# Optimization experiments

Measured on AMD Instinct MI355X. Metric: run time of the kernel, lower is better.

## Reference

```python
import jax
import jax.numpy as jnp
import numpy as np
from jax import lax

DELTA = float(np.exp(-2.0))  # rule-creation density threshold


def codebook_lamb(x):
    """Online growing RBF prototype codebook (ALMMo-style) for one layer.

    x: [N, M]. Returns lamb: [N] normalized density of each sample at its
    assigned rule. Faithful (corrected) semantics of Layer.__call__:
      - SEN = squared L2 norm per sample (over feature dim)
      - global mean / mean squared norm over the batch
      - sequential per-sample: if max RBF density over existing rules < exp(-2),
        append a new rule (prototype=c=x, SENc=||x||^2, support=1);
        else update rule_star. Note the source's `support[rule_star] = +1`
        assigns 1, so the running mean update degenerates to c[rule_star]=x,
        SENc[rule_star]=||x||^2 -- replicated here.
      - distances use the (never-updated) prototypes; bandwidth stau uses c.
    """
    N, M = x.shape
    SENx = jnp.sum(x * x, axis=-1)                      # [N]
    gmean = jnp.mean(x, axis=0)                         # [M]
    base = jnp.mean(SENx) - jnp.sum(gmean * gmean)      # SENgmean - SEN(gmean)
    R = N                                               # worst case: one rule/sample

    protos0 = jnp.zeros((R, M), x.dtype)
    pn20 = jnp.zeros((R,), x.dtype)                     # ||proto_r||^2 (carried)
    c0 = jnp.zeros((R, M), x.dtype)
    cn20 = jnp.zeros((R,), x.dtype)                     # ||c_r||^2 (carried)
    SENc0 = jnp.zeros((R,), x.dtype)
    count0 = jnp.int32(0)

    ridx = jnp.arange(R)

    def step(carry, inp):
        protos, pn2, c, cn2, SENc, count = carry
        xi, sxi = inp                                   # [M], scalar
        valid = ridx < count
        stau = (base + SENc - cn2) * 0.5                # [R]
        dist = sxi + pn2 - 2.0 * (protos @ xi)          # [R] ||xi - proto_r||^2
        dens = jnp.where(valid, jnp.exp(-dist / stau), -jnp.inf)
        idx = jnp.argmax(dens)
        vmax = dens[idx]
        new = (count == 0) | (vmax < DELTA)
        slot = jnp.where(new, count, idx)
        # both branches set c/SENc at slot to xi/sxi (support resets to 1)
        c = c.at[slot].set(xi)
        cn2 = cn2.at[slot].set(sxi)
        SENc = SENc.at[slot].set(sxi)
        # only a new rule writes a prototype (OOB scatter when count==R is dropped)
        protos = protos.at[count].set(jnp.where(new, xi, protos[count]))
        pn2 = pn2.at[count].set(jnp.where(new, sxi, pn2[count]))
        count = count + new.astype(count.dtype)
        return (protos, pn2, c, cn2, SENc, count), slot

    (protos, pn2, c, cn2, SENc, count), rules = lax.scan(
        step, (protos0, pn20, c0, cn20, SENc0, count0), (x, SENx)
    )

    # final densities of all samples under all (valid) rules: [R, N]
    stau = (base + SENc - cn2) * 0.5                    # [R]
    dist = SENx[None, :] + pn2[:, None] - 2.0 * (protos @ x.T)
    dens = jnp.where((ridx < count)[:, None], jnp.exp(-dist / stau[:, None]), 0.0)
    dens_xn = dens[rules, jnp.arange(N)]                # density at assigned rule
    lamb = dens_xn / jnp.sum(dens, axis=0)              # normalize over rules
    return lamb


def setup_inputs() -> dict:
    key = jax.random.key(0)
    k = jax.random.split(key, 5)
    N, D_IN, D_H, D_OUT = 2048, 2048, 2048, 1024
    s0 = 1.0 / np.sqrt(D_IN)
    s1 = 1.0 / np.sqrt(D_H)
    return {
        "x": jax.random.normal(k[0], (N, D_IN), jnp.float32),
        "W0": jax.random.normal(k[1], (D_H, D_IN), jnp.float32) * s0,
        "b0": jax.random.normal(k[2], (D_H,), jnp.float32) * s0,
        "W1": jax.random.normal(k[3], (D_OUT, D_H), jnp.float32) * s1,
        "b1": jax.random.normal(k[4], (D_OUT,), jnp.float32) * s1,
    }


def reference(x, W0, b0, W1, b1):
    lambs = []
    h = x
    for W, b in ((W0, b0), (W1, b1)):
        lambs.append(codebook_lamb(h))          # per-layer codebook on layer input
        h = jax.nn.sigmoid(h @ W.T + b)         # torch.nn.Linear + sigmoid
    return h, jnp.stack(lambs)                  # ([N, d_out], [n_layers, N])
```

## Files before the change

### kernel.cpp

```cpp
#include <hip/hip_runtime.h>
#include <cstdint>
#include <cstddef>


#define DELTA_F 0.13533528323661270f
#define MBYTE (1u << 20)

typedef __bf16 bf16;
typedef bf16 bf16x8 __attribute__((ext_vector_type(8)));
typedef bf16 bf16x4 __attribute__((ext_vector_type(4)));
typedef float f32x4 __attribute__((ext_vector_type(4)));

typedef __attribute__((address_space(1))) void as1_void;
typedef __attribute__((address_space(3))) void as3_void;

__device__ __forceinline__ void gload16(const bf16* g, bf16* l) {
  __builtin_amdgcn_global_load_lds((as1_void*)g, (as3_void*)l, 16, 0, 0);
}

__device__ __forceinline__ float wave_reduce(float s) {
  for (int o = 32; o > 0; o >>= 1) s += __shfl_down(s, o, 64);
  return s;
}

template <bool SAME>
__device__ void run_decide_lamb(char* smem, int* e, float* Dens, float* S,
                                float* diagD, float* lambOut) {
  char* s_flag = smem;
  short* s_as = (short*)(smem + 2048);
  short* s_list = (short*)(smem + 6144);
  short* s_re = (short*)(smem + 10240);
  int* scan_ = (int*)(smem + 14336);
  float* rbest = (float*)(smem + 16384);
  int* rbj = (int*)(smem + 18432);
  int* sT = (int*)(smem + 24576);
  int* sReN = (int*)(smem + 24580);
  const int tid = threadIdx.x;
  int cntl = 0;
#pragma unroll
  for (int k = 0; k < 4; ++k) {
    const int i = tid * 4 + k;
    const int ei = SAME ? atomicOr(e + i, 0) : e[i];
    s_flag[i] = (ei == 0);
    if (ei == 0) s_as[i] = (short)i;
    cntl += (ei != 0);
  }
  scan_[tid] = cntl;
  if (tid == 0) sReN[0] = 0;
  __syncthreads();
  for (int off = 1; off < 512; off <<= 1) {
    const int v = scan_[tid];
    const int add = (tid >= off) ? scan_[tid - off] : 0;
    __syncthreads();
    scan_[tid] = v + add;
    __syncthreads();
  }
  int pos = scan_[tid] - cntl;
#pragma unroll
  for (int k = 0; k < 4; ++k) {
    const int i = tid * 4 + k;
    if (!s_flag[i]) s_list[pos++] = (short)i;
  }
  if (tid == 511) sT[0] = scan_[511];
  __syncthreads();
  const int T = sT[0];
  if (SAME && T > 0) __threadfence();
  for (int t = 0; t < T; ++t) {
    const int i = s_list[t];
    const float* di = Dens + (size_t)i * 2048;
    float best = -1.0f;
    int bestj = 0x7fffffff;
    for (int j = tid; j < i; j += 512) {
      if (s_flag[j]) {
        const float d = di[j];
        if (d > best || (d == best && j < bestj)) { best = d; bestj = j; }
      }
    }
    rbest[tid] = best; rbj[tid] = bestj;
    __syncthreads();
    if (tid == 0) {
      float b = -1.0f;
      int bj = 0x7fffffff;
      for (int k = 0; k < 512; ++k)
        if (rbest[k] > b || (rbest[k] == b && rbj[k] < bj)) { b = rbest[k]; bj = rbj[k]; }
      if (b < DELTA_F) { s_flag[i] = 1; s_as[i] = (short)i; }
      else { s_as[i] = (short)bj; s_re[sReN[0]++] = (short)i; }
    }
    __syncthreads();
  }
  const int reN = sReN[0];
#pragma unroll
  for (int k = 0; k < 4; ++k) {
    const int n = k * 512 + tid;
    const int aa = s_as[n];
    const float num = (aa == n)
        ? (SAME ? atomicAdd(diagD + n, 0.f) : diagD[n])
        : Dens[(size_t)n * 2048 + aa];
    float denom = SAME ? atomicAdd(S + n, 0.f) : S[n];
    for (int t = 0; t < reN; ++t) denom -= Dens[(size_t)n * 2048 + s_re[t]];
    lambOut[n] = num / denom;
  }
}

template <bool IS_L0>
__global__ __launch_bounds__(512, 4) void gemm_fused(
    const bf16* __restrict__ A, float* __restrict__ Dens,
    bf16* __restrict__ Hb, float* __restrict__ Fo,
    const float* __restrict__ bias, const float* __restrict__ SENin,
    const float* __restrict__ ninv_p, float* __restrict__ S,
    int* __restrict__ e, float* __restrict__ SENhOut,
    float* __restrict__ colsumH, float* __restrict__ diagD,
    int* __restrict__ cnt, int nblocks, float* __restrict__ lambOut,
    int* __restrict__ flagN, const float* __restrict__ SENh_r,
    const float* __restrict__ colsumH_r, int* __restrict__ e0,
    float* __restrict__ S0, float* __restrict__ diag0,
    float* __restrict__ Dens0, float* __restrict__ lamb0) {
  __shared__ __align__(16) char smem[32768];
  __shared__ int s_last;
  const int tid = threadIdx.x;

  if (!IS_L0 && blockIdx.x == 24) {
    if (blockIdx.y != 0) return;
    float* r1 = (float*)(smem + 20480);
    float* r2 = (float*)(smem + 22528);
    float ssen = 0.f, sg2 = 0.f;
    for (int i = tid; i < 2048; i += 512) ssen += SENh_r[i];
    for (int c = tid; c < 2048; c += 512) {
      const float gm = colsumH_r[c] * (1.f / 2048.f);
      sg2 += gm * gm;
    }
    r1[tid] = ssen; r2[tid] = sg2;
    __syncthreads();
    for (int s = 256; s; s >>= 1) {
      if (tid < s) { r1[tid] += r1[tid + s]; r2[tid] += r2[tid + s]; }
      __syncthreads();
    }
    if (tid == 0) {
      const float stau = 0.5f * (r1[0] * (1.f / 2048.f) - r2[0]);
      atomicExch(flagN, __float_as_int(-1.f / stau));
    }
    __syncthreads();
    run_decide_lamb<false>(smem, e0, Dens0, S0, diag0, lamb0);
    return;
  }

  const int wave = tid >> 6, lane = tid & 63;
  const int quad = lane >> 4, l16 = lane & 15;
  const int kg = wave & 1, wm = (wave >> 1) & 1, wn = (wave >> 2) & 1;
  const int m0 = blockIdx.y * 128, n0 = blockIdx.x * 128;
  const int waveM = wm * 64, waveN = wn * 64;
  const bool isGram = (n0 < 2048);
  const int sr8 = lane >> 3, slot = lane & 7;
  const int gk = (slot ^ sr8) * 8;
  const bf16* aSrc = A + (size_t)(m0 + wave * 16 + sr8) * 2048 + gk;
  const bf16* bSrc = A + (size_t)(n0 + wave * 16 + sr8) * 2048 + gk;
  char* const aDst = smem + wave * 2048;
  char* const bDst = smem + 16384 + wave * 2048;
  const int swz = ((kg * 4 + quad) ^ (l16 & 7)) * 16;
  const int aOff = (waveM + l16) * 128 + swz;
  const int bOff = 16384 + (waveN + l16) * 128 + swz;

  f32x4 acc[4][4] = {};
  for (int k0 = 0; k0 < 2048; k0 += 64) {
    gload16(aSrc + k0, (bf16*)aDst);
    gload16(aSrc + 8 * 2048 + k0, (bf16*)(aDst + 1024));
    gload16(bSrc + k0, (bf16*)bDst);
    gload16(bSrc + 8 * 2048 + k0, (bf16*)(bDst + 1024));
    __syncthreads();
    bf16x8 af[4], bfr[4];
#pragma unroll
    for (int i = 0; i < 4; ++i) af[i] = *(const bf16x8*)(smem + aOff + i * 2048);
#pragma unroll
    for (int j = 0; j < 4; ++j) bfr[j] = *(const bf16x8*)(smem + bOff + j * 2048);
#pragma unroll
    for (int i = 0; i < 4; ++i)
#pragma unroll
      for (int j = 0; j < 4; ++j)
        acc[i][j] = __builtin_amdgcn_mfma_f32_16x16x32_bf16(af[i], bfr[j], acc[i][j], 0, 0, 0);
    __syncthreads();
  }

  float ninv = 0.f;
  if (isGram) {
    if (IS_L0) ninv = ninv_p[0];
    else {
      int fi;
      while ((fi = atomicOr(flagN, 0)) == 0) {}
      ninv = __int_as_float(fi);
    }
  }

  float colp[4] = {0.f, 0.f, 0.f, 0.f};
  char* const ex = smem + (wn * 2 + wm) * 8192;
#pragma unroll
  for (int round = 0; round < 2; ++round) {
    __syncthreads();
    if (kg == 1) {
#pragma unroll
      for (int ii = 0; ii < 2; ++ii)
#pragma unroll
        for (int j = 0; j < 4; ++j)
          *(f32x4*)(ex + (ii * 4 + j) * 1024 + lane * 16) = acc[round * 2 + ii][j];
    }
    __syncthreads();
    if (kg == 0) {
#pragma unroll
      for (int ii = 0; ii < 2; ++ii) {
        const int i = round * 2 + ii;
        const int rbase = m0 + waveM + i * 16 + quad * 4;
        if (isGram) {
          const f32x4 si4 = *(const f32x4*)(SENin + rbase);
          float rp[4] = {0.f, 0.f, 0.f, 0.f};
          int er = 0;
#pragma unroll
          for (int j = 0; j < 4; ++j) {
            f32x4 v = acc[i][j] + *(const f32x4*)(ex + (ii * 4 + j) * 1024 + lane * 16);
            const int col = n0 + waveN + j * 16 + l16;
            const float sj = SENin[col];
#pragma unroll
            for (int r = 0; r < 4; ++r) {
              const float dens = __expf((si4[r] + sj - 2.0f * v[r]) * ninv);
              Dens[(size_t)(rbase + r) * 2048 + col] = dens;
              rp[r] += dens;
              if (col < rbase + r && dens >= DELTA_F) er |= (1 << r);
              if (col == rbase + r) atomicExch(diagD + col, dens);
            }
          }
#pragma unroll
          for (int r = 0; r < 4; ++r) {
            float rv = rp[r];
            rv += __shfl_xor(rv, 1, 64); rv += __shfl_xor(rv, 2, 64);
            rv += __shfl_xor(rv, 4, 64); rv += __shfl_xor(rv, 8, 64);
            if (l16 == 0) atomicAdd(S + rbase + r, rv);
          }
          er |= __shfl_xor(er, 1, 64); er |= __shfl_xor(er, 2, 64);
          er |= __shfl_xor(er, 4, 64); er |= __shfl_xor(er, 8, 64);
          if (l16 == 0 && er) {
#pragma unroll
            for (int r = 0; r < 4; ++r)
              if ((er >> r) & 1) atomicOr(e + rbase + r, 1);
          }
        } else {
          float rn[4] = {0.f, 0.f, 0.f, 0.f};
#pragma unroll
          for (int j = 0; j < 4; ++j) {
            f32x4 v = acc[i][j] + *(const f32x4*)(ex + (ii * 4 + j) * 1024 + lane * 16);
            const int c2 = n0 - 2048 + waveN + j * 16 + l16;
            const float bv = bias[c2];
#pragma unroll
            for (int r = 0; r < 4; ++r) {
              const float hv = 1.0f / (1.0f + __expf(-(v[r] + bv)));
              if (IS_L0) {
                Hb[(size_t)(rbase + r) * 2048 + c2] = (bf16)hv;
                rn[r] += hv * hv;
                colp[j] += hv;
              } else {
                Fo[(size_t)(rbase + r) * 1024 + c2] = hv;
              }
            }
          }
          if (IS_L0) {
#pragma unroll
            for (int r = 0; r < 4; ++r) {
              float rv = rn[r];
              rv += __shfl_xor(rv, 1, 64); rv += __shfl_xor(rv, 2, 64);
              rv += __shfl_xor(rv, 4, 64); rv += __shfl_xor(rv, 8, 64);
              if (l16 == 0) atomicAdd(SENhOut + rbase + r, rv);
            }
          }
        }
      }
    }
  }
  if (IS_L0 && !isGram && kg == 0) {
#pragma unroll
    for (int j = 0; j < 4; ++j) {
      float cv = colp[j];
      cv += __shfl_xor(cv, 16, 64);
      cv += __shfl_xor(cv, 32, 64);
      if (lane < 16) atomicAdd(colsumH + (n0 - 2048 + waveN + j * 16 + lane), cv);
    }
  }

  if (IS_L0) return;

  __syncthreads();
  if (tid == 0) s_last = (atomicAdd(cnt, 1) == nblocks - 1);
  __syncthreads();
  if (!s_last) return;
  run_decide_lamb<true>(smem, e, Dens, S, diagD, lambOut);
}

__global__ void f2b_all(const float* __restrict__ x, const float* __restrict__ W0,
                        const float* __restrict__ W1, bf16* __restrict__ xb,
                        bf16* __restrict__ wb0, bf16* __restrict__ wb1,
                        float* __restrict__ SENx, float* __restrict__ bins,
                        int* __restrict__ cntF, float* __restrict__ scal) {
  const int b = blockIdx.x, tid = threadIdx.x;
  const int wave = tid >> 6, lane = tid & 63;
  __shared__ float ws[8][4];
  __shared__ float red1[256], red2[256];
  __shared__ int s_last;
  if (b < 256) {
    const int r0 = b * 8;
    f32x4 c0 = {0.f, 0.f, 0.f, 0.f}, c1 = {0.f, 0.f, 0.f, 0.f};
    for (int r = 0; r < 8; ++r) {
      const float* src = x + (size_t)(r0 + r) * 2048;
      bf16* dst = xb + (size_t)(r0 + r) * 2048;
      f32x4 v0 = *(const f32x4*)(src + tid * 4);
      f32x4 v1 = *(const f32x4*)(src + 1024 + tid * 4);
      bf16x4 o0, o1;
      o0.x = (bf16)v0.x; o0.y = (bf16)v0.y; o0.z = (bf16)v0.z; o0.w = (bf16)v0.w;
      o1.x = (bf16)v1.x; o1.y = (bf16)v1.y; o1.z = (bf16)v1.z; o1.w = (bf16)v1.w;
      *(bf16x4*)(dst + tid * 4) = o0;
      *(bf16x4*)(dst + 1024 + tid * 4) = o1;
      c0 += v0; c1 += v1;
      float rn = v0.x * v0.x + v0.y * v0.y + v0.z * v0.z + v0.w * v0.w +
                 v1.x * v1.x + v1.y * v1.y + v1.z * v1.z + v1.w * v1.w;
      rn = wave_reduce(rn);
      if (lane == 0) ws[r][wave] = rn;
    }
    __syncthreads();
    if (tid < 8)
      atomicExch(SENx + r0 + tid, ws[tid][0] + ws[tid][1] + ws[tid][2] + ws[tid][3]);
    float* bin = bins + (size_t)(b & 15) * 2048;
    atomicAdd(bin + tid * 4 + 0, c0.x); atomicAdd(bin + tid * 4 + 1, c0.y);
    atomicAdd(bin + tid * 4 + 2, c0.z); atomicAdd(bin + tid * 4 + 3, c0.w);
    atomicAdd(bin + 1024 + tid * 4 + 0, c1.x); atomicAdd(bin + 1024 + tid * 4 + 1, c1.y);
    atomicAdd(bin + 1024 + tid * 4 + 2, c1.z); atomicAdd(bin + 1024 + tid * 4 + 3, c1.w);
  } else if (b < 512) {
    const size_t base = (size_t)(b - 256) * 16384;
    for (int c = tid * 4; c < 16384; c += 1024) {
      f32x4 v = *(const f32x4*)(W0 + base + c);
      bf16x4 o;
      o.x = (bf16)v.x; o.y = (bf16)v.y; o.z = (bf16)v.z; o.w = (bf16)v.w;
      *(bf16x4*)(wb0 + base + c) = o;
    }
  } else {
    const size_t base = (size_t)(b - 512) * 16384;
    for (int c = tid * 4; c < 16384; c += 1024) {
      f32x4 v = *(const f32x4*)(W1 + base + c);
      bf16x4 o;
      o.x = (bf16)v.x; o.y = (bf16)v.y; o.z = (bf16)v.z; o.w = (bf16)v.w;
      *(bf16x4*)(wb1 + base + c) = o;
    }
  }

  __syncthreads();
  if (tid == 0) s_last = (atomicAdd(cntF, 1) == 639);
  __syncthreads();
  if (!s_last) return;
  float ssen = 0.f;
  for (int i = tid; i < 2048; i += 256) ssen += atomicAdd(SENx + i, 0.f);
  float sg2 = 0.f;
  for (int c = tid; c < 2048; c += 256) {
    float cs = 0.f;
#pragma unroll
    for (int p = 0; p < 16; ++p) cs += atomicAdd(bins + (size_t)p * 2048 + c, 0.f);
    const float gm = cs * (1.f / 2048.f);
    sg2 += gm * gm;
  }
  red1[tid] = ssen; red2[tid] = sg2;
  __syncthreads();
  for (int s = 128; s; s >>= 1) {
    if (tid < s) { red1[tid] += red1[tid + s]; red2[tid] += red2[tid + s]; }
    __syncthreads();
  }
  if (tid == 0) {
    const float stau = 0.5f * (red1[0] * (1.f / 2048.f) - red2[0]);
    scal[0] = stau;
    scal[1] = -1.f / stau;
  }
}

extern "C" void kernel_launch(void* const* d_in, const int* in_sizes, int n_in,
                              void* d_out, int out_size, void* d_ws, size_t ws_size,
                              hipStream_t stream) {
  const float* x = (const float*)d_in[0];
  const float* W0 = (const float*)d_in[1];
  const float* b0 = (const float*)d_in[2];
  const float* W1 = (const float*)d_in[3];
  const float* b1 = (const float*)d_in[4];
  float* out = (float*)d_out;

  char* w = (char*)d_ws;
  bf16* xb = (bf16*)(w);
  bf16* wb0 = (bf16*)(w + 8 * MBYTE);
  bf16* hb = (bf16*)(w + 16 * MBYTE);
  bf16* wb1 = (bf16*)(w + 24 * MBYTE);
  float* Dens0 = (float*)(w + 28 * MBYTE);
  float* Dens1 = (float*)(w);
  float* SENx = (float*)(w + 44 * MBYTE);
  float* scal = SENx + 2048;
  float* zre = scal + 16;
  float* bins = zre;
  float* SENh = bins + 16 * 2048;
  float* colsumH = SENh + 2048;
  float* S0 = colsumH + 2048;
  float* S1 = S0 + 2048;
  float* diagD0 = S1 + 2048;
  float* diagD1 = diagD0 + 2048;
  int* e0 = (int*)(diagD1 + 2048);
  int* e1 = e0 + 2048;
  int* cntF = e1 + 2048;
  int* cnt1 = cntF + 1;
  int* flagN = cnt1 + 1;
  const size_t zwords = 16 * 2048 + 8 * 2048 + 16;

  float* lamb0 = out + (size_t)2048 * 1024;
  float* lamb1 = lamb0 + 2048;

  hipMemsetAsync(zre, 0, zwords * 4, stream);
  f2b_all<<<640, 256, 0, stream>>>(x, W0, W1, xb, wb0, wb1, SENx, bins, cntF, scal);
  gemm_fused<true><<<dim3(32, 16), 512, 0, stream>>>(
      xb, Dens0, hb, nullptr, b0, SENx, scal + 1, S0, e0, SENh, colsumH,
      diagD0, nullptr, 0, nullptr,
      nullptr, nullptr, nullptr, nullptr, nullptr, nullptr, nullptr, nullptr);
  gemm_fused<false><<<dim3(25, 16), 512, 0, stream>>>(
      hb, Dens1, nullptr, out, b1, SENh, nullptr, S1, e1, nullptr, nullptr,
      diagD1, cnt1, 384, lamb1,
      flagN, SENh, colsumH, e0, S0, diagD0, Dens0, lamb0);
}
```

Baseline: 192.5 us.

## Double-buffer LDS tiles in the fused GEMM main loop

```diff
diff --git a/kernel.cpp b/kernel.cpp
--- a/kernel.cpp
+++ b/kernel.cpp
@@ -115,14 +115,15 @@
     const float* __restrict__ colsumH_r, int* __restrict__ e0,
     float* __restrict__ S0, float* __restrict__ diag0,
     float* __restrict__ Dens0, float* __restrict__ lamb0) {
-  __shared__ __align__(16) char smem[32768];
+  __shared__ __align__(16) char smemA[32768];
+  __shared__ __align__(16) char smemB[32768];
   __shared__ int s_last;
   const int tid = threadIdx.x;
 
   if (!IS_L0 && blockIdx.x == 24) {
     if (blockIdx.y != 0) return;
-    float* r1 = (float*)(smem + 20480);
-    float* r2 = (float*)(smem + 22528);
+    float* r1 = (float*)(smemA + 20480);
+    float* r2 = (float*)(smemA + 22528);
     float ssen = 0.f, sg2 = 0.f;
     for (int i = tid; i < 2048; i += 512) ssen += SENh_r[i];
     for (int c = tid; c < 2048; c += 512) {
@@ -140,7 +141,7 @@
       atomicExch(flagN, __float_as_int(-1.f / stau));
     }
     __syncthreads();
-    run_decide_lamb<false>(smem, e0, Dens0, S0, diag0, lamb0);
+    run_decide_lamb<false>(smemA, e0, Dens0, S0, diag0, lamb0);
     return;
   }
 
@@ -154,31 +155,47 @@
   const int gk = (slot ^ sr8) * 8;
   const bf16* aSrc = A + (size_t)(m0 + wave * 16 + sr8) * 2048 + gk;
   const bf16* bSrc = A + (size_t)(n0 + wave * 16 + sr8) * 2048 + gk;
-  char* const aDst = smem + wave * 2048;
-  char* const bDst = smem + 16384 + wave * 2048;
+  char* const aDst0 = smemA + wave * 2048;
+  char* const bDst0 = smemA + 16384 + wave * 2048;
+  char* const aDst1 = smemB + wave * 2048;
+  char* const bDst1 = smemB + 16384 + wave * 2048;
   const int swz = ((kg * 4 + quad) ^ (l16 & 7)) * 16;
   const int aOff = (waveM + l16) * 128 + swz;
   const int bOff = 16384 + (waveN + l16) * 128 + swz;
 
+#define STAGE(aD, bD, k)                              \
+  do {                                                \
+    gload16(aSrc + (k), (bf16*)(aD));                 \
+    gload16(aSrc + 8 * 2048 + (k), (bf16*)((aD) + 1024)); \
+    gload16(bSrc + (k), (bf16*)(bD));                 \
+    gload16(bSrc + 8 * 2048 + (k), (bf16*)((bD) + 1024)); \
+  } while (0)
+
+#define COMPUTE(sm)                                                        \
+  do {                                                                     \
+    bf16x8 af[4], bfr[4];                                                  \
+    _Pragma("unroll") for (int i = 0; i < 4; ++i)                          \
+        af[i] = *(const bf16x8*)((sm) + aOff + i * 2048);                  \
+    _Pragma("unroll") for (int j = 0; j < 4; ++j)                          \
+        bfr[j] = *(const bf16x8*)((sm) + bOff + j * 2048);                 \
+    _Pragma("unroll") for (int i = 0; i < 4; ++i)                          \
+        _Pragma("unroll") for (int j = 0; j < 4; ++j) acc[i][j] =          \
+            __builtin_amdgcn_mfma_f32_16x16x32_bf16(af[i], bfr[j],         \
+                                                    acc[i][j], 0, 0, 0);   \
+  } while (0)
+
   f32x4 acc[4][4] = {};
-  for (int k0 = 0; k0 < 2048; k0 += 64) {
-    gload16(aSrc + k0, (bf16*)aDst);
-    gload16(aSrc + 8 * 2048 + k0, (bf16*)(aDst + 1024));
-    gload16(bSrc + k0, (bf16*)bDst);
-    gload16(bSrc + 8 * 2048 + k0, (bf16*)(bDst + 1024));
-    __syncthreads();
-    bf16x8 af[4], bfr[4];
-#pragma unroll
-    for (int i = 0; i < 4; ++i) af[i] = *(const bf16x8*)(smem + aOff + i * 2048);
-#pragma unroll
-    for (int j = 0; j < 4; ++j) bfr[j] = *(const bf16x8*)(smem + bOff + j * 2048);
-#pragma unroll
-    for (int i = 0; i < 4; ++i)
-#pragma unroll
-      for (int j = 0; j < 4; ++j)
-        acc[i][j] = __builtin_amdgcn_mfma_f32_16x16x32_bf16(af[i], bfr[j], acc[i][j], 0, 0, 0);
-    __syncthreads();
-  }
+  STAGE(aDst0, bDst0, 0);
+  for (int k0 = 0; k0 < 2048; k0 += 128) {
+    __syncthreads();
+    STAGE(aDst1, bDst1, k0 + 64);
+    COMPUTE(smemA);
+    __syncthreads();
+    if (k0 + 128 < 2048) STAGE(aDst0, bDst0, k0 + 128);
+    COMPUTE(smemB);
+  }
+#undef STAGE
+#undef COMPUTE
 
   float ninv = 0.f;
   if (isGram) {
@@ -191,7 +208,7 @@
   }
 
   float colp[4] = {0.f, 0.f, 0.f, 0.f};
-  char* const ex = smem + (wn * 2 + wm) * 8192;
+  char* const ex = smemA + (wn * 2 + wm) * 8192;
 #pragma unroll
   for (int round = 0; round < 2; ++round) {
     __syncthreads();
@@ -288,7 +305,7 @@
   if (tid == 0) s_last = (atomicAdd(cnt, 1) == nblocks - 1);
   __syncthreads();
   if (!s_last) return;
-  run_decide_lamb<true>(smem, e, Dens, S, diagD, lambOut);
+  run_decide_lamb<true>(smemA, e, Dens, S, diagD, lambOut);
 }
 
 __global__ void f2b_all(const float* __restrict__ x, const float* __restrict__ W0,
```

Measured after the change: 190.0 us. No clear change (-1.3%).
